# Performance work log

Measured on AMD Instinct MI355X. Metric: run time of the kernel, lower is better.

The kernel has to match this reference:

```python
import jax, jax.numpy as jnp
import numpy as np

LOW_T = 25.5   # 0.1 * 255
HIGH_T = 76.5  # 0.3 * 255


def _dwconv3x3(img, k):
    # img: [B, C, H, W]; k: [3, 3]; depthwise conv with replicate border (as OpenCV Sobel)
    B, C, H, W = img.shape
    p = jnp.pad(img, ((0, 0), (0, 0), (1, 1), (1, 1)), mode='edge')
    kern = jnp.broadcast_to(k.astype(img.dtype), (C, 1, 3, 3))
    return jax.lax.conv_general_dilated(p, kern, (1, 1), 'VALID', feature_group_count=C)


def _shift(a, dy, dx):
    # a: [B, H, W]; shift by (dy, dx), zero at out-of-range borders
    B, H, W = a.shape
    p = jnp.pad(a, ((0, 0), (1, 1), (1, 1)))
    return p[:, 1 + dy:1 + dy + H, 1 + dx:1 + dx + W]


def canny(x, low, high):
    # x: [B, 3, H, W] in [0, 1]
    B, C, H, W = x.shape
    img = jnp.floor(jnp.clip(x, 0.0, 1.0) * 255.0)  # uint8 quantization, kept float

    kx = jnp.array([[-1., 0., 1.], [-2., 0., 2.], [-1., 0., 1.]])
    ky = jnp.array([[-1., -2., -1.], [0., 0., 0.], [1., 2., 1.]])
    gx = _dwconv3x3(img, kx)  # [B, C, H, W]
    gy = _dwconv3x3(img, ky)

    # L1 gradient magnitude (OpenCV default L2gradient=False); multi-channel:
    # pick the channel with max magnitude per pixel (OpenCV behavior)
    mag_c = jnp.abs(gx) + jnp.abs(gy)                      # [B, C, H, W]
    idx = jnp.argmax(mag_c, axis=1, keepdims=True)         # [B, 1, H, W]
    gxs = jnp.take_along_axis(gx, idx, axis=1)[:, 0]       # [B, H, W]
    gys = jnp.take_along_axis(gy, idx, axis=1)[:, 0]
    mag = jnp.take_along_axis(mag_c, idx, axis=1)[:, 0]

    # Non-maximum suppression: quantize gradient direction into 4 bins
    PI = np.float32(np.pi)
    ang = jnp.mod(jnp.arctan2(gys, gxs), PI)               # [0, pi)
    b = (jnp.floor((ang + PI / 8) / (PI / 4)).astype(jnp.int32)) % 4  # [B, H, W]

    # neighbor offsets along gradient direction per bin: 0deg, 45deg, 90deg, 135deg
    offs = [((0, 1), (0, -1)), ((1, 1), (-1, -1)), ((1, 0), (-1, 0)), ((1, -1), (-1, 1))]
    s1 = jnp.stack([_shift(mag, dy, dx) for (dy, dx), _ in offs])   # [4, B, H, W]
    s2 = jnp.stack([_shift(mag, dy, dx) for _, (dy, dx) in offs])
    n1 = jnp.take_along_axis(s1, b[None], axis=0)[0]
    n2 = jnp.take_along_axis(s2, b[None], axis=0)[0]
    nms = jnp.where((mag >= n1) & (mag >= n2), mag, 0.0)

    # Double threshold + hysteresis (8-connected propagation to fixed point)
    strong = (nms > high).astype(x.dtype)
    weak = (nms > low).astype(x.dtype)

    def cond(c):
        return c[1]

    def body(c):
        s, _ = c
        d = jax.lax.reduce_window(s, 0.0, jax.lax.max, (1, 3, 3), (1, 1, 1), 'SAME')
        ns = jnp.maximum(s, d * weak)
        return ns, jnp.any(ns != s)

    edges, _ = jax.lax.while_loop(cond, body, (strong, jnp.array(True)))

    # cv2.cvtColor GRAY2RGB then /255 -> {0, 1} replicated over 3 channels
    return jnp.broadcast_to(edges[:, None], (B, C, H, W))


def setup_inputs() -> dict:
    key = jax.random.key(0)
    x = jax.random.uniform(key, (16, 3, 720, 1280), dtype=jnp.float32)
    return {"x": x}


def reference(x):
    return canny(x, LOW_T, HIGH_T)
```

## Files before the change

### kernel.cpp

```cpp
#include <hip/hip_runtime.h>
#include <hip/hip_cooperative_groups.h>
#include <stdint.h>

namespace cg = cooperative_groups;
typedef unsigned long long u64;

static constexpr int BB  = 16;
static constexpr int HH  = 720;
static constexpr int WW  = 1280;
static constexpr int HWP = HH * WW;
static constexpr int WORDS_X = WW / 64;
static constexpr long long OUT_ELEMS = (long long)BB * 3 * HWP;
static constexpr size_t OUT_BYTES = (size_t)OUT_ELEMS * 4;
static constexpr size_t PLANE_B = (size_t)BB * HH * WORDS_X * 8;
static constexpr int N16 = (int)(OUT_ELEMS / 16);
static constexpr int KGRID = 512;
static constexpr int KNT = KGRID * 256;
static constexpr int OSLOT = (N16 + KNT - 1) / KNT;

typedef short v4s __attribute__((ext_vector_type(4)));
union QW { u64 u; v4s v; };

__device__ __forceinline__ int dirbin_b(int gx, int gy)
{
    int u  = (gy < 0) ? -gx : gx;
    int vv = gy < 0 ? -gy : gy;
    int A  = u < 0 ? -u : u;
    int b2 = 2 * A * A;
    int tt = vv + A;
    int dd = vv - A;
    bool P1 = (tt * tt < b2);
    bool P2 = (dd < 0) || (dd * dd < b2);
    return P1 ? 0 : (P2 ? ((u > 0) ? 1 : 3) : 2);
}

__global__ __launch_bounds__(256)
void k_gradnms(const float* __restrict__ x, u64* __restrict__ splane,
               u64* __restrict__ wplane)
{
    __shared__ __align__(16) u64 qimg[20][72];
    __shared__ int mtile[18][68];

    const int blk = blockIdx.x;
    const int bx = blk % 20;
    const int t1 = blk / 20;
    const int by = t1 % 45;
    const int b  = t1 / 45;
    const int x0 = bx << 6, y0 = by << 4;
    const float* bp = x + (size_t)b * 3 * HWP;

    for (int i = threadIdx.x; i < 20 * 34; i += 256) {
        int r   = i / 34;
        int pc  = i - r * 34;
        int col = pc * 2;
        int gy = y0 - 2 + r;   gy = gy < 0 ? 0 : (gy > HH - 1 ? HH - 1 : gy);
        int gx = x0 - 2 + col;
        const float* row = bp + (size_t)gy * WW;
        float a0, a1, b0, b1, c0, c1;
        if (gx >= 0 && gx + 1 < WW) {
            float2 fa = *(const float2*)(row + gx);
            float2 fb = *(const float2*)(row + HWP + gx);
            float2 fc = *(const float2*)(row + 2 * HWP + gx);
            a0 = fa.x; a1 = fa.y; b0 = fb.x; b1 = fb.y; c0 = fc.x; c1 = fc.y;
        } else {
            int g0 = gx     < 0 ? 0 : (gx     > WW - 1 ? WW - 1 : gx);
            int g1 = gx + 1 < 0 ? 0 : (gx + 1 > WW - 1 ? WW - 1 : gx + 1);
            a0 = row[g0];           a1 = row[g1];
            b0 = row[HWP + g0];     b1 = row[HWP + g1];
            c0 = row[2 * HWP + g0]; c1 = row[2 * HWP + g1];
        }
        uint32_t qa0 = (uint32_t)(fminf(fmaxf(a0, 0.f), 1.f) * 255.f);
        uint32_t qb0 = (uint32_t)(fminf(fmaxf(b0, 0.f), 1.f) * 255.f);
        uint32_t qc0 = (uint32_t)(fminf(fmaxf(c0, 0.f), 1.f) * 255.f);
        uint32_t qa1 = (uint32_t)(fminf(fmaxf(a1, 0.f), 1.f) * 255.f);
        uint32_t qb1 = (uint32_t)(fminf(fmaxf(b1, 0.f), 1.f) * 255.f);
        uint32_t qc1 = (uint32_t)(fminf(fmaxf(c1, 0.f), 1.f) * 255.f);
        ulonglong2 wv;
        wv.x = (u64)(qa0 | (qb0 << 16)) | ((u64)qc0 << 32);
        wv.y = (u64)(qa1 | (qb1 << 16)) | ((u64)qc1 << 32);
        *(ulonglong2*)&qimg[r][col] = wv;
    }
    __syncthreads();

    if (threadIdx.x < 18 * 14) {
        int r  = threadIdx.x / 14;
        int g  = threadIdx.x - r * 14;
        int c0 = g * 5;
        int my = y0 - 1 + r;
        bool rowok = (my >= 0 && my < HH);
        v4s s[7], t[7];
#pragma unroll
        for (int k = 0; k < 7; ++k) {
            QW w0, w1, w2;
            w0.u = qimg[r    ][c0 + k];
            w1.u = qimg[r + 1][c0 + k];
            w2.u = qimg[r + 2][c0 + k];
            s[k] = w0.v + w1.v + w1.v + w2.v;
            t[k] = w2.v - w0.v;
        }
        int mx0 = x0 - 1 + c0;
#pragma unroll
        for (int j = 0; j < 5; ++j) {
            int c = c0 + j;
            if (c >= 66) continue;
            int pk = 0;
            int mx = mx0 + j;
            if (rowok && mx >= 0 && mx < WW) {
                v4s gx4 = s[j + 2] - s[j];
                v4s gy4 = t[j] + t[j + 1] + t[j + 1] + t[j + 2];
                v4s ax = __builtin_elementwise_max(gx4, -gx4);
                v4s ay = __builtin_elementwise_max(gy4, -gy4);
                QW mq; mq.v = ax + ay;
                int m0 = (int)(mq.u & 0xffffull);
                int m1 = (int)((mq.u >> 16) & 0xffffull);
                int m2 = (int)((mq.u >> 32) & 0xffffull);
                int bm = m0, bi = 0;
                if (m1 > bm) { bm = m1; bi = 1; }
                if (m2 > bm) { bm = m2; bi = 2; }
                QW gq; gq.v = gx4;
                QW hq; hq.v = gy4;
                int sh = bi << 4;
                int bgx = (int)(short)(gq.u >> sh);
                int bgy = (int)(short)(hq.u >> sh);
                pk = bm | (dirbin_b(bgx, bgy) << 12);
            }
            mtile[r][c] = pk;
        }
    }
    __syncthreads();

    const int v = threadIdx.x >> 6, l = threadIdx.x & 63;
#pragma unroll
    for (int k = 0; k < 4; ++k) {
        int ry = v * 4 + k;
        int pk = mtile[ry + 1][l + 1];
        int m = pk & 0xFFF, bin = pk >> 12;
        int dy = (bin == 0) ? 0 : 1;
        int dx = (bin == 2) ? 0 : ((bin == 3) ? -1 : 1);
        int n1 = mtile[ry + 1 + dy][l + 1 + dx] & 0xFFF;
        int n2 = mtile[ry + 1 - dy][l + 1 - dx] & 0xFFF;
        int keep = (m >= n1) && (m >= n2);
        u64 sB = __ballot(keep && m >= 77);
        u64 wB = __ballot(keep && m >= 26);
        if (l == 0) {
            size_t rb = ((size_t)b * HH + (y0 + ry)) * WORDS_X + bx;
            splane[rb] = sB;
            wplane[rb] = wB;
        }
    }
}

__device__ __forceinline__ u64 sh_up(u64 x, int k) {
    int l = threadIdx.x & 63;
    u64 y = __shfl(x, l - k, 64);
    return (l >= k) ? y : 0ull;
}
__device__ __forceinline__ u64 sh_dn(u64 x, int k) {
    int l = threadIdx.x & 63;
    u64 y = __shfl(x, l + k, 64);
    return (l + k < 64) ? y : 0ull;
}
__device__ __forceinline__ u64 dil(u64 x) { return x | (x << 1) | (x >> 1); }

__device__ __forceinline__ u64 hflood_L(u64 f, u64 w) {
    u64 p = w;
    f |= p & (f << 1);  p &= (p << 1);
    f |= p & (f << 2);  p &= (p << 2);
    f |= p & (f << 4);  p &= (p << 4);
    f |= p & (f << 8);  p &= (p << 8);
    f |= p & (f << 16); p &= (p << 16);
    f |= p & (f << 32);
    return f;
}
__device__ __forceinline__ u64 hflood_R(u64 f, u64 w) {
    u64 p = w;
    f |= p & (f >> 1);  p &= (p >> 1);
    f |= p & (f >> 2);  p &= (p >> 2);
    f |= p & (f >> 4);  p &= (p >> 4);
    f |= p & (f >> 8);  p &= (p >> 8);
    f |= p & (f >> 16); p &= (p >> 16);
    f |= p & (f >> 32);
    return f;
}

__global__ __launch_bounds__(768, 3)
void k_hyst_local(u64* __restrict__ splane, const u64* __restrict__ wplane)
{
    __shared__ u64 sTop[12][20], sBot[12][20];
    __shared__ int schg[2];

    const int b = blockIdx.x;
    const int r = threadIdx.x;
    const int l = threadIdx.x & 63;
    const int v = threadIdx.x >> 6;
    const bool valid = r < HH;
    const size_t base = ((size_t)b * HH + (valid ? r : 0)) * WORDS_X;

    u64 W[20], F[20];
#pragma unroll
    for (int j = 0; j < 20; ++j) {
        W[j] = valid ? wplane[base + j] : 0ull;
        F[j] = valid ? splane[base + j] : 0ull;
    }

    auto converge_band = [&]() {
        while (true) {
            u64 carry = 0;
#pragma unroll
            for (int j = 0; j < 20; ++j) {
                u64 f = F[j] | (W[j] & carry);
                f = hflood_L(f, W[j]);
                F[j] = f;
                carry = (f >> 63) & 1ull;
            }
            carry = 0;
#pragma unroll
            for (int j = 19; j >= 0; --j) {
                u64 f = F[j] | (W[j] & (carry << 63));
                f = hflood_R(f, W[j]);
                F[j] = f;
                carry = f & 1ull;
            }
            int ch = 0;
            u64 po = 0;
            u64 cur = F[0];
#pragma unroll
            for (int j = 0; j < 20; ++j) {
                u64 nx = (j < 19) ? F[j + 1] : 0ull;
                u64 n = dil(cur) | ((po >> 63) & 1ull) | ((nx & 1ull) << 63);
                po = cur; cur = nx;
                u64 add = W[j] & (sh_up(n, 1) | sh_dn(n, 1)) & ~F[j];
                ch |= (add != 0ull);
                F[j] |= add;
            }
            if (!__any(ch)) break;
        }
    };

    if (threadIdx.x == 0) { schg[0] = 0; schg[1] = 0; }
    converge_band();

    int iter = 0;
    while (true) {
        const int c = iter & 1;
        if (threadIdx.x == 0) schg[c ^ 1] = 0;

        if (l == 0 || l == 63) {
#pragma unroll
            for (int j = 0; j < 20; ++j) {
                u64 d = dil(F[j]);
                if (j > 0)  d |= (F[j-1] >> 63) & 1ull;
                if (j < 19) d |= (F[j+1] & 1ull) << 63;
                if (l == 0) sTop[v][j] = d; else sBot[v][j] = d;
            }
        }
        __syncthreads();

        int anynb = 0;
#pragma unroll
        for (int j = 0; j < 20; ++j) {
            u64 s = 0ull;
            if (l == 0  && v > 0)  s = sBot[v-1][j];
            else if (l == 63 && v < 11) s = sTop[v+1][j];
            u64 add = W[j] & s & ~F[j];
            anynb |= (add != 0ull);
            F[j] |= add;
        }
        if (__any(anynb)) {
            converge_band();
            schg[c] = 1;
        }
        __syncthreads();
        if (!schg[c]) break;
        ++iter;
    }

#pragma unroll
    for (int j = 0; j < 20; ++j)
        if (valid) splane[base + j] = F[j];
}

__global__ __launch_bounds__(256)
void k_out(const u64* __restrict__ splane, float* __restrict__ out)
{
    int i = blockIdx.x * 256 + threadIdx.x;
    int px  = i * 16;
    int bb  = px / (3 * HWP);
    int rem = px - bb * (3 * HWP);
    int yx  = rem % HWP;
    int y   = yx / WW;
    int xx  = yx - y * WW;
    u64 wv = splane[((size_t)bb * HH + y) * WORDS_X + (xx >> 6)];
    uint32_t bits = (uint32_t)((wv >> (xx & 63)) & 0xFFFFull);
    float4* o4 = (float4*)(out + (size_t)i * 16);
#pragma unroll
    for (int q = 0; q < 4; ++q) {
        float4 fv;
        fv.x = (bits >> (q * 4 + 0)) & 1 ? 1.0f : 0.0f;
        fv.y = (bits >> (q * 4 + 1)) & 1 ? 1.0f : 0.0f;
        fv.z = (bits >> (q * 4 + 2)) & 1 ? 1.0f : 0.0f;
        fv.w = (bits >> (q * 4 + 3)) & 1 ? 1.0f : 0.0f;
        o4[q] = fv;
    }
}

__global__ __launch_bounds__(256, 4)
void k_out_capture(const u64* __restrict__ splane, float* __restrict__ out)
{
    cg::grid_group grid = cg::this_grid();
    const int gtid = blockIdx.x * 256 + threadIdx.x;
    uint32_t vals[OSLOT];
#pragma unroll
    for (int n = 0; n < OSLOT; ++n) {
        int i = gtid + n * KNT;
        if (i < N16) {
            int px  = i * 16;
            int bb  = px / (3 * HWP);
            int rem = px - bb * (3 * HWP);
            int yx  = rem % HWP;
            int y   = yx / WW;
            int xx  = yx - y * WW;
            u64 wv = splane[((size_t)bb * HH + y) * WORDS_X + (xx >> 6)];
            vals[n] = (uint32_t)((wv >> (xx & 63)) & 0xFFFFull);
        }
    }
    grid.sync();
#pragma unroll
    for (int n = 0; n < OSLOT; ++n) {
        int i = gtid + n * KNT;
        if (i < N16) {
            uint32_t bits = vals[n];
            float4* o4 = (float4*)(out + (size_t)i * 16);
#pragma unroll
            for (int q = 0; q < 4; ++q) {
                float4 fv;
                fv.x = (bits >> (q * 4 + 0)) & 1 ? 1.0f : 0.0f;
                fv.y = (bits >> (q * 4 + 1)) & 1 ? 1.0f : 0.0f;
                fv.z = (bits >> (q * 4 + 2)) & 1 ? 1.0f : 0.0f;
                fv.w = (bits >> (q * 4 + 3)) & 1 ? 1.0f : 0.0f;
                o4[q] = fv;
            }
        }
    }
}

extern "C" void kernel_launch(void* const* d_in, const int* in_sizes, int n_in,
                              void* d_out, int out_size, void* d_ws, size_t ws_size,
                              hipStream_t stream)
{
    const float* x = (const float*)d_in[0];
    float* out = (float*)d_out;

    const bool use_ws = (d_ws != nullptr) && (ws_size >= 2 * PLANE_B);
    u64 *splane, *wplane;
    if (use_ws) {
        splane = (u64*)d_ws;
        wplane = (u64*)((char*)d_ws + PLANE_B);
    } else {
        char* tail = (char*)d_out + OUT_BYTES;
        wplane = (u64*)(tail - PLANE_B);
        splane = (u64*)(tail - 2 * PLANE_B);
    }

    k_gradnms<<<20 * 45 * BB, 256, 0, stream>>>(x, splane, wplane);
    k_hyst_local<<<BB, 768, 0, stream>>>(splane, wplane);

    if (use_ws) {
        k_out<<<N16 / 256, 256, 0, stream>>>(splane, out);
    } else {
        void* args[] = { (void*)&splane, (void*)&out };
        hipLaunchCooperativeKernel((void*)k_out_capture, dim3(KGRID), dim3(256),
                                   args, 0, stream);
    }
}
```

Before: 207.9 us.

## Process two image rows per thread in hysteresis kernel with 384-thread blocks

The hysteresis kernel now gives each thread two adjacent rows, so one block uses 6 wavefronts of 64 lanes (128 rows each) instead of 12. The two rows inside a thread propagate to each other directly in registers, which halves the number of band boundaries exchanged through shared memory and the number of waves taking part in the block barrier. In exchange each thread carries twice the register state, and the serial per-thread work per sweep doubles, which could limit overlap since only 16 blocks run.

Measured after the change: 332.4 us. +59.9%, slower.

```diff
diff --git a/kernel.cpp b/kernel.cpp
--- a/kernel.cpp
+++ b/kernel.cpp
@@ -183,55 +183,76 @@
     return f;
 }
 
-__global__ __launch_bounds__(768, 3)
-void k_hyst_local(u64* __restrict__ splane, const u64* __restrict__ wplane)
-{
-    __shared__ u64 sTop[12][20], sBot[12][20];
+__global__ __launch_bounds__(384, 1)
+void k_hyst_pair(u64* __restrict__ splane, const u64* __restrict__ wplane)
+{
+    __shared__ u64 sTop[6][20], sBot[6][20];
     __shared__ int schg[2];
 
     const int b = blockIdx.x;
-    const int r = threadIdx.x;
     const int l = threadIdx.x & 63;
     const int v = threadIdx.x >> 6;
-    const bool valid = r < HH;
-    const size_t base = ((size_t)b * HH + (valid ? r : 0)) * WORDS_X;
-
-    u64 W[20], F[20];
+    const int r0 = 128 * v + 2 * l;
+    const int r1 = r0 + 1;
+    const bool val0 = r0 < HH;
+    const bool val1 = r1 < HH;
+    const size_t base0 = ((size_t)b * HH + (val0 ? r0 : 0)) * WORDS_X;
+    const size_t base1 = ((size_t)b * HH + (val1 ? r1 : 0)) * WORDS_X;
+
+    u64 W0[20], W1[20], F0[20], F1[20];
 #pragma unroll
     for (int j = 0; j < 20; ++j) {
-        W[j] = valid ? wplane[base + j] : 0ull;
-        F[j] = valid ? splane[base + j] : 0ull;
+        W0[j] = val0 ? wplane[base0 + j] : 0ull;
+        F0[j] = val0 ? splane[base0 + j] : 0ull;
+        W1[j] = val1 ? wplane[base1 + j] : 0ull;
+        F1[j] = val1 ? splane[base1 + j] : 0ull;
     }
 
     auto converge_band = [&]() {
         while (true) {
-            u64 carry = 0;
-#pragma unroll
-            for (int j = 0; j < 20; ++j) {
-                u64 f = F[j] | (W[j] & carry);
-                f = hflood_L(f, W[j]);
-                F[j] = f;
-                carry = (f >> 63) & 1ull;
-            }
-            carry = 0;
+            u64 cr = 0;
+#pragma unroll
+            for (int j = 0; j < 20; ++j) {
+                u64 f = F0[j] | (W0[j] & cr);
+                f = hflood_L(f, W0[j]);
+                F0[j] = f; cr = (f >> 63) & 1ull;
+            }
+            cr = 0;
 #pragma unroll
             for (int j = 19; j >= 0; --j) {
-                u64 f = F[j] | (W[j] & (carry << 63));
-                f = hflood_R(f, W[j]);
-                F[j] = f;
-                carry = f & 1ull;
+                u64 f = F0[j] | (W0[j] & (cr << 63));
+                f = hflood_R(f, W0[j]);
+                F0[j] = f; cr = f & 1ull;
+            }
+            cr = 0;
+#pragma unroll
+            for (int j = 0; j < 20; ++j) {
+                u64 f = F1[j] | (W1[j] & cr);
+                f = hflood_L(f, W1[j]);
+                F1[j] = f; cr = (f >> 63) & 1ull;
+            }
+            cr = 0;
+#pragma unroll
+            for (int j = 19; j >= 0; --j) {
+                u64 f = F1[j] | (W1[j] & (cr << 63));
+                f = hflood_R(f, W1[j]);
+                F1[j] = f; cr = f & 1ull;
             }
             int ch = 0;
-            u64 po = 0;
-            u64 cur = F[0];
-#pragma unroll
-            for (int j = 0; j < 20; ++j) {
-                u64 nx = (j < 19) ? F[j + 1] : 0ull;
-                u64 n = dil(cur) | ((po >> 63) & 1ull) | ((nx & 1ull) << 63);
-                po = cur; cur = nx;
-                u64 add = W[j] & (sh_up(n, 1) | sh_dn(n, 1)) & ~F[j];
-                ch |= (add != 0ull);
-                F[j] |= add;
+#pragma unroll
+            for (int j = 0; j < 20; ++j) {
+                u64 d1 = dil(F1[j]);
+                if (j > 0)  d1 |= (F1[j - 1] >> 63) & 1ull;
+                if (j < 19) d1 |= (F1[j + 1] & 1ull) << 63;
+                u64 add0 = W0[j] & (d1 | sh_up(d1, 1)) & ~F0[j];
+                u64 f0 = F0[j] | add0;
+                u64 d0 = dil(f0);
+                if (j > 0)  d0 |= (F0[j - 1] >> 63) & 1ull;
+                if (j < 19) d0 |= (F0[j + 1] & 1ull) << 63;
+                u64 add1 = W1[j] & (d0 | sh_dn(d0, 1)) & ~F1[j];
+                ch |= ((add0 | add1) != 0ull);
+                F0[j] = f0;
+                F1[j] |= add1;
             }
             if (!__any(ch)) break;
         }
@@ -245,26 +266,42 @@
         const int c = iter & 1;
         if (threadIdx.x == 0) schg[c ^ 1] = 0;
 
-        if (l == 0 || l == 63) {
-#pragma unroll
-            for (int j = 0; j < 20; ++j) {
-                u64 d = dil(F[j]);
-                if (j > 0)  d |= (F[j-1] >> 63) & 1ull;
-                if (j < 19) d |= (F[j+1] & 1ull) << 63;
-                if (l == 0) sTop[v][j] = d; else sBot[v][j] = d;
+        if (l == 0) {
+#pragma unroll
+            for (int j = 0; j < 20; ++j) {
+                u64 d = dil(F0[j]);
+                if (j > 0)  d |= (F0[j - 1] >> 63) & 1ull;
+                if (j < 19) d |= (F0[j + 1] & 1ull) << 63;
+                sTop[v][j] = d;
+            }
+        }
+        if (l == 63) {
+#pragma unroll
+            for (int j = 0; j < 20; ++j) {
+                u64 d = dil(F1[j]);
+                if (j > 0)  d |= (F1[j - 1] >> 63) & 1ull;
+                if (j < 19) d |= (F1[j + 1] & 1ull) << 63;
+                sBot[v][j] = d;
             }
         }
         __syncthreads();
 
         int anynb = 0;
-#pragma unroll
-        for (int j = 0; j < 20; ++j) {
-            u64 s = 0ull;
-            if (l == 0  && v > 0)  s = sBot[v-1][j];
-            else if (l == 63 && v < 11) s = sTop[v+1][j];
-            u64 add = W[j] & s & ~F[j];
-            anynb |= (add != 0ull);
-            F[j] |= add;
+        if (l == 0 && v > 0) {
+#pragma unroll
+            for (int j = 0; j < 20; ++j) {
+                u64 add = W0[j] & sBot[v - 1][j] & ~F0[j];
+                anynb |= (add != 0ull);
+                F0[j] |= add;
+            }
+        }
+        if (l == 63 && v < 5) {
+#pragma unroll
+            for (int j = 0; j < 20; ++j) {
+                u64 add = W1[j] & sTop[v + 1][j] & ~F1[j];
+                anynb |= (add != 0ull);
+                F1[j] |= add;
+            }
         }
         if (__any(anynb)) {
             converge_band();
@@ -276,8 +313,10 @@
     }
 
 #pragma unroll
-    for (int j = 0; j < 20; ++j)
-        if (valid) splane[base + j] = F[j];
+    for (int j = 0; j < 20; ++j) {
+        if (val0) splane[base0 + j] = F0[j];
+        if (val1) splane[base1 + j] = F1[j];
+    }
 }
 
 __global__ __launch_bounds__(256)
@@ -363,7 +402,7 @@
     }
 
     k_gradnms<<<20 * 45 * BB, 256, 0, stream>>>(x, splane, wplane);
-    k_hyst_local<<<BB, 768, 0, stream>>>(splane, wplane);
+    k_hyst_pair<<<BB, 384, 0, stream>>>(splane, wplane);
 
     if (use_ws) {
         k_out<<<N16 / 256, 256, 0, stream>>>(splane, out);
```
